# Kernel optimization log

Measured on AMD Instinct MI355X. Metric: run time of the kernel, lower is better.

Reference implementation:

```python
import jax, jax.numpy as jnp
import numpy as np

H, W = 128, 128
FOCAL_X = FOCAL_Y = 128.0
NEAR = 0.3
N_GAUSS = 2048
EPS = 1e-4  # regularizer on 2D covariance diagonal


def q2r(q):
    """Quaternion (w,x,y,z) [N,4] -> rotation matrices [N,3,3]."""
    q = q / jnp.linalg.norm(q, axis=-1, keepdims=True)
    w, x, y, z = q[:, 0], q[:, 1], q[:, 2], q[:, 3]
    R = jnp.stack([
        1 - 2 * (y * y + z * z), 2 * (x * y - w * z), 2 * (x * z + w * y),
        2 * (x * y + w * z), 1 - 2 * (x * x + z * z), 2 * (y * z - w * x),
        2 * (x * z - w * y), 2 * (y * z + w * x), 1 - 2 * (x * x + y * y),
    ], axis=-1).reshape(-1, 3, 3)
    return R


def setup_inputs():
    key = jax.random.key(0)
    ks = jax.random.split(key, 6)
    # gaussians placed inside the camera frustum (camera looks along +z)
    xy = jax.random.uniform(ks[0], (N_GAUSS, 2), minval=-1.5, maxval=1.5)
    z = jax.random.uniform(ks[1], (N_GAUSS, 1), minval=2.0, maxval=6.0)
    pos = jnp.concatenate([xy * z / 4.0, z], axis=-1)
    rgb = jax.random.normal(ks[2], (N_GAUSS, 3))
    opa = jax.random.normal(ks[3], (N_GAUSS,))
    quat = jax.random.normal(ks[4], (N_GAUSS, 4))
    scale = jax.random.uniform(ks[5], (N_GAUSS, 3), minval=0.01, maxval=0.05)
    ang = 0.05  # small camera rotation about y
    rot = jnp.array([[np.cos(ang), 0.0, np.sin(ang)],
                     [0.0, 1.0, 0.0],
                     [-np.sin(ang), 0.0, np.cos(ang)]], dtype=jnp.float32)
    tran = jnp.array([0.0, 0.0, 0.1], dtype=jnp.float32)
    return {"pos": pos, "rgb": rgb, "opa": opa, "quat": quat,
            "scale": scale, "rot": rot, "tran": tran}


def _forward(pos, rgb, opa, quat, scale, rot, tran):
    # ---- project: world -> camera -> image space (Gaussian3ds.project) ----
    pos_cam = pos @ rot.T + tran                       # [N,3]
    x, y, z = pos_cam[:, 0], pos_cam[:, 1], pos_cam[:, 2]
    r = jnp.linalg.norm(pos_cam, axis=-1)              # depth = ||p_cam||
    u, v = x / z, y / z                                # normalized image coords
    zero = jnp.zeros_like(z)
    # jacobian of (x/z, y/z, ||p||) wrt camera coords (jacobian_torch)
    J = jnp.stack([1.0 / z, zero, -x / (z * z),
                   zero, 1.0 / z, -y / (z * z),
                   x / r, y / r, z / r], axis=-1).reshape(-1, 3, 3)
    # 3D covariance: R S S^T R^T with abs scale activation
    Rm = q2r(quat)
    s = jnp.abs(scale) + 1e-4
    RS = Rm * s[:, None, :]                            # R @ diag(s)
    cov3d = jnp.einsum('nij,nkj->nik', RS, RS)
    JW = jnp.einsum('nij,jk->nik', J, rot)
    cov2d = jnp.einsum('nij,njk,nlk->nil', JW, cov3d, JW)[:, :2, :2]
    a = cov2d[:, 0, 0] + EPS
    b = cov2d[:, 0, 1]
    c = cov2d[:, 1, 1] + EPS
    det = a * c - b * b
    ia, ib, ic = c / det, -b / det, a / det            # inverse 2x2 cov entries
    rgb_s = jax.nn.sigmoid(rgb)
    opa_s = jax.nn.sigmoid(opa)
    # ---- global front-to-back depth sort ----
    order = jnp.argsort(r)
    u, v = u[order], v[order]
    ia, ib, ic = ia[order], ib[order], ic[order]
    opa_s, zs = opa_s[order], z[order]
    rgb_s = rgb_s[order]
    # ---- alpha composite over all pixels (tiles merged -> dense) ----
    px = (jnp.arange(W) - W / 2 + 0.5) / FOCAL_X
    py = (jnp.arange(H) - H / 2 + 0.5) / FOCAL_Y
    yy, xx = jnp.meshgrid(py, px, indexing='ij')
    pxf, pyf = xx.reshape(-1), yy.reshape(-1)          # [P]
    dx = pxf[:, None] - u[None, :]                     # [P,N]
    dy = pyf[:, None] - v[None, :]
    power = -0.5 * (ia * dx * dx + 2.0 * ib * dx * dy + ic * dy * dy)
    alpha = jnp.clip(opa_s * jnp.exp(power), 0.0, 0.99)
    alpha = alpha * (zs > NEAR)                        # near-plane cull as mask
    T = jnp.cumprod(1.0 - alpha, axis=1)
    T_excl = jnp.concatenate([jnp.ones((T.shape[0], 1), T.dtype), T[:, :-1]], axis=1)
    img = (T_excl * alpha) @ rgb_s                     # [P,3]
    return img.reshape(H, W, 3)


def reference(pos, rgb, opa, quat, scale, rot, tran):
    return _forward(pos, rgb, opa, quat, scale, rot, tran)
```

## Files before the change

kernel.cpp:

```cpp
#include <hip/hip_runtime.h>
#include <hip/hip_bf16.h>

#define NG     2048
#define HW     128
#define NPIX   (HW*HW)
#define SEG    16
#define CHUNK  (NG/SEG)
#define NEARZ  0.3f
#define GEPS   1e-4f
#define LOG2E  1.4426950408889634f

__device__ float4 g_ga_s[NG];
__device__ float4 g_gb_s[NG];
__device__ float  g_cb_s[NG];

__device__ __forceinline__ float sigm(float x) { return 1.0f / (1.0f + __expf(-x)); }

__device__ __forceinline__ bool detect_f32(const void* rot) {
    return ((const unsigned short*)rot)[1] != 0;
}
__device__ __forceinline__ float ld(const void* p, int idx, bool f32) {
    if (f32) return ((const float*)p)[idx];
    return __bfloat162float(((const __hip_bfloat16*)p)[idx]);
}

__global__ __launch_bounds__(256)
void prep_sort_kernel(const void* __restrict__ pos,
                      const void* __restrict__ rgb,
                      const void* __restrict__ opa,
                      const void* __restrict__ quat,
                      const void* __restrict__ scale,
                      const void* __restrict__ rot,
                      const void* __restrict__ tran)
{
    __shared__ float rs[NG];
    __shared__ int   srank[16];

    int tid = threadIdx.x;
    bool f32 = detect_f32(rot);

    float R[9], T3[3];
    #pragma unroll
    for (int k = 0; k < 9; k++) R[k] = ld(rot, k, f32);
    #pragma unroll
    for (int k = 0; k < 3; k++) T3[k] = ld(tran, k, f32);

    #pragma unroll
    for (int k = 0; k < NG / 256; k++) {
        int j = tid + k * 256;
        float p0 = ld(pos, j*3+0, f32), p1 = ld(pos, j*3+1, f32), p2 = ld(pos, j*3+2, f32);
        float x = R[0]*p0 + R[1]*p1 + R[2]*p2 + T3[0];
        float y = R[3]*p0 + R[4]*p1 + R[5]*p2 + T3[1];
        float z = R[6]*p0 + R[7]*p1 + R[8]*p2 + T3[2];
        rs[j] = sqrtf(x*x + y*y + z*z);
    }
    __syncthreads();

    int g      = blockIdx.x * 16 + (tid >> 4);
    int lane16 = tid & 15;
    float ri = rs[g];
    int rank = 0;
    int jbase = lane16 * CHUNK;
    #pragma unroll 4
    for (int jj = 0; jj < CHUNK; jj++) {
        int j = jbase + ((jj + 2 * lane16) & (CHUNK - 1));
        float rj = rs[j];
        rank += (rj < ri) || (rj == ri && j < g);
    }
    #pragma unroll
    for (int d = 1; d < 16; d <<= 1) rank += __shfl_xor(rank, d);
    if (lane16 == 0) srank[tid >> 4] = rank;
    __syncthreads();

    if (tid < 16) {
        int i = blockIdx.x * 16 + tid;
        int rk = srank[tid];

        float p0 = ld(pos, i*3+0, f32), p1 = ld(pos, i*3+1, f32), p2 = ld(pos, i*3+2, f32);
        float x = R[0]*p0 + R[1]*p1 + R[2]*p2 + T3[0];
        float y = R[3]*p0 + R[4]*p1 + R[5]*p2 + T3[1];
        float z = R[6]*p0 + R[7]*p1 + R[8]*p2 + T3[2];
        float iz = 1.0f / z;
        float u = x * iz, v = y * iz;

        float qw = ld(quat, i*4+0, f32), qx = ld(quat, i*4+1, f32);
        float qy = ld(quat, i*4+2, f32), qz = ld(quat, i*4+3, f32);
        float qn = 1.0f / sqrtf(qw*qw + qx*qx + qy*qy + qz*qz);
        qw *= qn; qx *= qn; qy *= qn; qz *= qn;
        float Rm[3][3];
        Rm[0][0] = 1.0f - 2.0f*(qy*qy + qz*qz);
        Rm[0][1] = 2.0f*(qx*qy - qw*qz);
        Rm[0][2] = 2.0f*(qx*qz + qw*qy);
        Rm[1][0] = 2.0f*(qx*qy + qw*qz);
        Rm[1][1] = 1.0f - 2.0f*(qx*qx + qz*qz);
        Rm[1][2] = 2.0f*(qy*qz - qw*qx);
        Rm[2][0] = 2.0f*(qx*qz - qw*qy);
        Rm[2][1] = 2.0f*(qy*qz + qw*qx);
        Rm[2][2] = 1.0f - 2.0f*(qx*qx + qy*qy);

        float s[3];
        #pragma unroll
        for (int k = 0; k < 3; k++) s[k] = fabsf(ld(scale, i*3+k, f32)) + 1e-4f;

        float RS[3][3];
        #pragma unroll
        for (int a = 0; a < 3; a++)
            #pragma unroll
            for (int b = 0; b < 3; b++) RS[a][b] = Rm[a][b] * s[b];
        float C3[3][3];
        #pragma unroll
        for (int a = 0; a < 3; a++)
            #pragma unroll
            for (int b = 0; b < 3; b++)
                C3[a][b] = RS[a][0]*RS[b][0] + RS[a][1]*RS[b][1] + RS[a][2]*RS[b][2];

        float nx = -x * iz * iz, ny = -y * iz * iz;
        float jw0[3], jw1[3];
        #pragma unroll
        for (int k = 0; k < 3; k++) {
            jw0[k] = iz * R[0*3+k] + nx * R[2*3+k];
            jw1[k] = iz * R[1*3+k] + ny * R[2*3+k];
        }
        float t0[3], t1[3];
        #pragma unroll
        for (int j = 0; j < 3; j++) {
            t0[j] = C3[j][0]*jw0[0] + C3[j][1]*jw0[1] + C3[j][2]*jw0[2];
            t1[j] = C3[j][0]*jw1[0] + C3[j][1]*jw1[1] + C3[j][2]*jw1[2];
        }
        float a = jw0[0]*t0[0] + jw0[1]*t0[1] + jw0[2]*t0[2] + GEPS;
        float b = jw0[0]*t1[0] + jw0[1]*t1[1] + jw0[2]*t1[2];
        float c = jw1[0]*t1[0] + jw1[1]*t1[1] + jw1[2]*t1[2] + GEPS;
        float idet = 1.0f / (a*c - b*b);
        float Af = -0.5f * LOG2E * (c * idet);
        float Bf = -LOG2E * (-b * idet);
        float Cf = -0.5f * LOG2E * (a * idet);

        float om = (z > NEARZ) ? sigm(ld(opa, i, f32)) : 0.0f;
        float cr = sigm(ld(rgb, i*3+0, f32));
        float cg = sigm(ld(rgb, i*3+1, f32));
        float cb = sigm(ld(rgb, i*3+2, f32));

        g_ga_s[rk] = make_float4(u, v, Af, Bf);
        g_gb_s[rk] = make_float4(Cf, om, cr, cg);
        g_cb_s[rk] = cb;
    }
}

__global__ __launch_bounds__(1024)
void raster_kernel(void* __restrict__ out, const void* __restrict__ rot)
{
    __shared__ float4 comb[SEG * 64];

    int tid  = threadIdx.x;
    int lane = tid & 63;
    int w    = __builtin_amdgcn_readfirstlane(tid >> 6);

    int pix = blockIdx.x * 64 + lane;
    int row = pix >> 7;
    int col = pix & 127;
    float pxf = (col - 63.5f) * (1.0f / 128.0f);
    float pyf = (row - 63.5f) * (1.0f / 128.0f);

    float T = 1.0f, Cr = 0.0f, Cg = 0.0f, Cb = 0.0f;
    int base = w * CHUNK;
    #pragma unroll 8
    for (int k = 0; k < CHUNK; k++) {
        float4 a4 = g_ga_s[base + k];
        float4 b4 = g_gb_s[base + k];
        float  cb = g_cb_s[base + k];
        float dx = pxf - a4.x;
        float dy = pyf - a4.y;
        float p  = (a4.z * dx + a4.w * dy) * dx;
        p = fmaf(b4.x * dy, dy, p);
        float alpha = fminf(b4.y * __builtin_amdgcn_exp2f(p), 0.99f);
        float wgt = T * alpha;
        Cr = fmaf(wgt, b4.z, Cr);
        Cg = fmaf(wgt, b4.w, Cg);
        Cb = fmaf(wgt, cb, Cb);
        T -= wgt;
    }

    comb[w * 64 + lane] = make_float4(T, Cr, Cg, Cb);
    __syncthreads();

    if (tid < 64) {
        float Ta = 1.0f, Ra = 0.0f, Ga = 0.0f, Ba = 0.0f;
        #pragma unroll
        for (int s = 0; s < SEG; s++) {
            float4 c4 = comb[s * 64 + lane];
            Ra = fmaf(Ta, c4.y, Ra);
            Ga = fmaf(Ta, c4.z, Ga);
            Ba = fmaf(Ta, c4.w, Ba);
            Ta *= c4.x;
        }
        if (detect_f32(rot)) {
            float* o = (float*)out;
            o[pix*3 + 0] = Ra; o[pix*3 + 1] = Ga; o[pix*3 + 2] = Ba;
        } else {
            __hip_bfloat16* o = (__hip_bfloat16*)out;
            o[pix*3 + 0] = __float2bfloat16(Ra);
            o[pix*3 + 1] = __float2bfloat16(Ga);
            o[pix*3 + 2] = __float2bfloat16(Ba);
        }
    }
}

extern "C" void kernel_launch(void* const* d_in, const int* in_sizes, int n_in,
                              void* d_out, int out_size, void* d_ws, size_t ws_size,
                              hipStream_t stream)
{
    const void* pos   = d_in[0];
    const void* rgb   = d_in[1];
    const void* opa   = d_in[2];
    const void* quat  = d_in[3];
    const void* scale = d_in[4];
    const void* rot   = d_in[5];
    const void* tran  = d_in[6];

    prep_sort_kernel<<<NG/16, 256, 0, stream>>>(pos, rgb, opa, quat, scale, rot, tran);
    raster_kernel<<<NPIX/64, 1024, 0, stream>>>(d_out, rot);
}
```

Baseline: 97.19 us.

## Cull gaussians per wave row-segment using precomputed screen-space bounding boxes

The prep kernel now computes a 6.5-sigma screen-space bounding box for each gaussian from the largest eigenvalue of its 2D covariance and packs it into a 32-bit word. In the raster kernel each wave ballots over 64 gaussians at a time and only evaluates those whose box overlaps its 64-pixel row segment. This removes most exp and blend work, since the gaussians are small. In exchange it adds ballot and bit-iteration overhead, and contributions beyond 6.5 sigma are dropped as an approximation.

```diff
diff --git a/kernel.cpp b/kernel.cpp
--- a/kernel.cpp
+++ b/kernel.cpp
@@ -10,9 +10,10 @@
 #define GEPS   1e-4f
 #define LOG2E  1.4426950408889634f
 
-__device__ float4 g_ga_s[NG];
-__device__ float4 g_gb_s[NG];
-__device__ float  g_cb_s[NG];
+__device__ float4   g_ga_s[NG];
+__device__ float4   g_gb_s[NG];
+__device__ float    g_cb_s[NG];
+__device__ unsigned g_bb_s[NG];
 
 __device__ __forceinline__ float sigm(float x) { return 1.0f / (1.0f + __expf(-x)); }
 
@@ -73,7 +74,7 @@
     __syncthreads();
 
     if (tid < 16) {
-        int i = blockIdx.x * 16 + tid;
+        int i  = blockIdx.x * 16 + tid;
         int rk = srank[tid];
 
         float p0 = ld(pos, i*3+0, f32), p1 = ld(pos, i*3+1, f32), p2 = ld(pos, i*3+2, f32);
@@ -130,7 +131,8 @@
         float a = jw0[0]*t0[0] + jw0[1]*t0[1] + jw0[2]*t0[2] + GEPS;
         float b = jw0[0]*t1[0] + jw0[1]*t1[1] + jw0[2]*t1[2];
         float c = jw1[0]*t1[0] + jw1[1]*t1[1] + jw1[2]*t1[2] + GEPS;
-        float idet = 1.0f / (a*c - b*b);
+        float det  = a*c - b*b;
+        float idet = 1.0f / det;
         float Af = -0.5f * LOG2E * (c * idet);
         float Bf = -LOG2E * (-b * idet);
         float Cf = -0.5f * LOG2E * (a * idet);
@@ -140,9 +142,28 @@
         float cg = sigm(ld(rgb, i*3+1, f32));
         float cb = sigm(ld(rgb, i*3+2, f32));
 
+        float mid = 0.5f * (a + c);
+        float lam = mid + sqrtf(fmaxf(mid*mid - det, 0.0f));
+        float rad = 6.5f * sqrtf(lam) * 128.0f;
+        float u_px = u * 128.0f + 63.5f;
+        float v_px = v * 128.0f + 63.5f;
+        unsigned bb = 0xFF00FF00u;
+        if (om > 0.0f) {
+            int ymn = (int)ceilf (v_px - rad);
+            int ymx = (int)floorf(v_px + rad);
+            int xmn = (int)ceilf (u_px - rad);
+            int xmx = (int)floorf(u_px + rad);
+            if (ymx >= 0 && ymn <= 127 && xmx >= 0 && xmn <= 127) {
+                ymn = max(ymn, 0); ymx = min(ymx, 127);
+                xmn = max(xmn, 0); xmx = min(xmx, 127);
+                bb = (unsigned)((ymn << 24) | (ymx << 16) | (xmn << 8) | xmx);
+            }
+        }
+
         g_ga_s[rk] = make_float4(u, v, Af, Bf);
         g_gb_s[rk] = make_float4(Cf, om, cr, cg);
         g_cb_s[rk] = cb;
+        g_bb_s[rk] = bb;
     }
 }
 
@@ -156,28 +177,44 @@
     int w    = __builtin_amdgcn_readfirstlane(tid >> 6);
 
     int pix = blockIdx.x * 64 + lane;
-    int row = pix >> 7;
-    int col = pix & 127;
+    int row = blockIdx.x >> 1;
+    int x0  = (blockIdx.x & 1) * 64;
+    int x1  = x0 + 63;
+    int col = x0 + lane;
     float pxf = (col - 63.5f) * (1.0f / 128.0f);
     float pyf = (row - 63.5f) * (1.0f / 128.0f);
 
     float T = 1.0f, Cr = 0.0f, Cg = 0.0f, Cb = 0.0f;
     int base = w * CHUNK;
-    #pragma unroll 8
-    for (int k = 0; k < CHUNK; k++) {
-        float4 a4 = g_ga_s[base + k];
-        float4 b4 = g_gb_s[base + k];
-        float  cb = g_cb_s[base + k];
-        float dx = pxf - a4.x;
-        float dy = pyf - a4.y;
-        float p  = (a4.z * dx + a4.w * dy) * dx;
-        p = fmaf(b4.x * dy, dy, p);
-        float alpha = fminf(b4.y * __builtin_amdgcn_exp2f(p), 0.99f);
-        float wgt = T * alpha;
-        Cr = fmaf(wgt, b4.z, Cr);
-        Cg = fmaf(wgt, b4.w, Cg);
-        Cb = fmaf(wgt, cb, Cb);
-        T -= wgt;
+
+    #pragma unroll
+    for (int c = 0; c < CHUNK / 64; c++) {
+        int cbase = base + c * 64;
+        unsigned bb = g_bb_s[cbase + lane];
+        int ymn =  bb >> 24;
+        int ymx = (bb >> 16) & 255;
+        int xmn = (bb >>  8) & 255;
+        int xmx =  bb        & 255;
+        bool hit = (row >= ymn) & (row <= ymx) & (x1 >= xmn) & (x0 <= xmx);
+        unsigned long long m = __ballot(hit);
+        while (m) {
+            int kk = __builtin_ctzll(m);
+            m &= m - 1;
+            int idx = cbase + kk;
+            float4 a4 = g_ga_s[idx];
+            float4 b4 = g_gb_s[idx];
+            float  cc = g_cb_s[idx];
+            float dx = pxf - a4.x;
+            float dy = pyf - a4.y;
+            float p  = (a4.z * dx + a4.w * dy) * dx;
+            p = fmaf(b4.x * dy, dy, p);
+            float alpha = fminf(b4.y * __builtin_amdgcn_exp2f(p), 0.99f);
+            float wgt = T * alpha;
+            Cr = fmaf(wgt, b4.z, Cr);
+            Cg = fmaf(wgt, b4.w, Cg);
+            Cb = fmaf(wgt, cc, Cb);
+            T -= wgt;
+        }
     }
 
     comb[w * 64 + lane] = make_float4(T, Cr, Cg, Cb);
```

After: 90.17 us, median of 2. -7.2%, faster.
